# Kernel optimization log

Hardware: AMD Instinct MI355X
Metric: run time of the kernel (lower is better)

The kernel has to match this reference:

```python
import jax, jax.numpy as jnp
import numpy as np

N_USERS = 100000
N_ITEMS = 200000
N_TOTAL = N_USERS + N_ITEMS
N_EDGES = 6000000
D = 64


def setup_inputs() -> dict:
    key = jax.random.key(0)
    ks = jax.random.split(key, 7)
    A_row = jax.random.randint(ks[0], (N_EDGES,), 0, N_TOTAL, dtype=jnp.int32)
    A_col = jax.random.randint(ks[1], (N_EDGES,), 0, N_TOTAL, dtype=jnp.int32)
    A_val = jax.random.uniform(ks[2], (N_EDGES,), dtype=jnp.float32)
    user_feat = jax.random.normal(ks[3], (N_USERS, D), dtype=jnp.float32)
    item_feat = jax.random.normal(ks[4], (N_ITEMS, D), dtype=jnp.float32)
    W = jax.random.normal(ks[5], (D, D), dtype=jnp.float32) * (6.0 / (D + D)) ** 0.5
    b = jnp.zeros((D,), dtype=jnp.float32)
    return {"A_row": A_row, "A_col": A_col, "A_val": A_val,
            "user_feat": user_feat, "item_feat": item_feat, "W": W, "b": b}


def reference(A_row, A_col, A_val, user_feat, item_feat, W, b):
    # fc applied to users and items (same weight), then concat -> [N_total, D]
    all_feat = jnp.concatenate([user_feat, item_feat], axis=0)
    trans = all_feat @ W.T + b  # nn.Linear: x @ W^T + b
    # sparse A (COO) @ trans: gather source rows, scale by edge value, scatter-add to dest
    msgs = A_val[:, None] * trans[A_col]  # [E, D]
    conv = jax.ops.segment_sum(msgs, A_row, num_segments=N_TOTAL)  # [N_total, D]
    # identity residual (in_dim == out_dim)
    out = conv + all_feat
    return out[:N_USERS], out[N_USERS:]
```

## Files before the change

kernel.cpp:

```cpp
#include <hip/hip_runtime.h>
#include <hip/hip_fp16.h>

#define N_USERS 100000
#define N_ITEMS 200000
#define N_TOTAL 300000
#define N_EDGES 6000000
#define D 64

#define B2SHIFT 10
#define B2ROWS 1024
#define NBUCK2 ((N_TOTAL + B2ROWS - 1) / B2ROWS)
#define CAP 22016
#define EPB 8192
#define NPB ((N_EDGES + EPB - 1) / EPB)

#define VSCALE 8191.0f
#define VINV   (1.0f / 8191.0f)

typedef float    f32x4 __attribute__((ext_vector_type(4)));
typedef float    f32x2 __attribute__((ext_vector_type(2)));
typedef _Float16 f16x8 __attribute__((ext_vector_type(8)));

#define LIN_BLOCKS ((N_TOTAL + 63) / 64)

__global__ __launch_bounds__(256) void fused_lin_part_kernel(
    const float* __restrict__ user_feat,
    const float* __restrict__ item_feat,
    const float* __restrict__ W,
    const float* __restrict__ bias,
    __half* __restrict__ trans,
    const int*   __restrict__ A_row,
    const int*   __restrict__ A_col,
    const float* __restrict__ A_val,
    int*  __restrict__ gcur,
    int2* __restrict__ kv)
{
    if (blockIdx.x < NPB) {
        __shared__ int lcnt[NBUCK2];
        __shared__ int gb[NBUCK2];
        for (int i = threadIdx.x; i < NBUCK2; i += 256) lcnt[i] = 0;
        __syncthreads();

        const int base = blockIdx.x * EPB;
        int pk[32];
        #pragma unroll
        for (int j = 0; j < 8; ++j) {
            const int e0 = base + j * 1024 + threadIdx.x * 4;
            if (e0 < N_EDGES) {
                const int4 r = *reinterpret_cast<const int4*>(A_row + e0);
                pk[4*j+0] = ((r.x >> B2SHIFT) << 13) | atomicAdd(&lcnt[r.x >> B2SHIFT], 1);
                pk[4*j+1] = ((r.y >> B2SHIFT) << 13) | atomicAdd(&lcnt[r.y >> B2SHIFT], 1);
                pk[4*j+2] = ((r.z >> B2SHIFT) << 13) | atomicAdd(&lcnt[r.z >> B2SHIFT], 1);
                pk[4*j+3] = ((r.w >> B2SHIFT) << 13) | atomicAdd(&lcnt[r.w >> B2SHIFT], 1);
            }
        }
        __syncthreads();
        for (int i = threadIdx.x; i < NBUCK2; i += 256)
            gb[i] = lcnt[i] ? atomicAdd(&gcur[i], lcnt[i]) : 0;
        __syncthreads();

        #pragma unroll
        for (int j = 0; j < 8; ++j) {
            const int e0 = base + j * 1024 + threadIdx.x * 4;
            if (e0 < N_EDGES) {
                const int4   r = *reinterpret_cast<const int4*>(A_row + e0);
                const int4   c = *reinterpret_cast<const int4*>(A_col + e0);
                const float4 v = *reinterpret_cast<const float4*>(A_val + e0);
                const int rr[4] = {r.x, r.y, r.z, r.w};
                const int cc[4] = {c.x, c.y, c.z, c.w};
                const float vv[4] = {v.x, v.y, v.z, v.w};
                #pragma unroll
                for (int q = 0; q < 4; ++q) {
                    const int p   = pk[4*j+q];
                    const int bk  = p >> 13;
                    const int pos = gb[bk] + (p & 0x1FFF);
                    if (pos < CAP) {
                        kv[(size_t)bk * CAP + pos] = make_int2(
                            ((rr[q] & (B2ROWS - 1)) << 19) | cc[q],
                            __float_as_int(vv[q]));
                    }
                }
            }
        }
    } else {
        const int bid  = blockIdx.x - NPB;
        const int lane = threadIdx.x & 63;
        const int wv   = threadIdx.x >> 6;
        const int r0   = bid * 64 + wv * 16;
        const int arow = lane & 15;
        const int kg   = lane >> 4;

        f16x8 wf[4][2];
        #pragma unroll
        for (int ct = 0; ct < 4; ++ct) {
            const float* wp = W + (size_t)(ct * 16 + arow) * D;
            #pragma unroll
            for (int kf = 0; kf < 2; ++kf) {
                const int k0 = kf * 32 + kg * 8;
                const float4 w0 = *reinterpret_cast<const float4*>(wp + k0);
                const float4 w1 = *reinterpret_cast<const float4*>(wp + k0 + 4);
                f16x8 h;
                h[0] = (_Float16)w0.x; h[1] = (_Float16)w0.y;
                h[2] = (_Float16)w0.z; h[3] = (_Float16)w0.w;
                h[4] = (_Float16)w1.x; h[5] = (_Float16)w1.y;
                h[6] = (_Float16)w1.z; h[7] = (_Float16)w1.w;
                wf[ct][kf] = h;
            }
        }

        int rr = r0 + arow;
        if (rr >= N_TOTAL) rr = N_TOTAL - 1;
        const float* fp = (rr < N_USERS) ? user_feat + (size_t)rr * D
                                         : item_feat + (size_t)(rr - N_USERS) * D;
        f16x8 af[2];
        #pragma unroll
        for (int kf = 0; kf < 2; ++kf) {
            const int k0 = kf * 32 + kg * 8;
            const float4 a0 = *reinterpret_cast<const float4*>(fp + k0);
            const float4 a1 = *reinterpret_cast<const float4*>(fp + k0 + 4);
            f16x8 h;
            h[0] = (_Float16)a0.x; h[1] = (_Float16)a0.y;
            h[2] = (_Float16)a0.z; h[3] = (_Float16)a0.w;
            h[4] = (_Float16)a1.x; h[5] = (_Float16)a1.y;
            h[6] = (_Float16)a1.z; h[7] = (_Float16)a1.w;
            af[kf] = h;
        }

        #pragma unroll
        for (int ct = 0; ct < 4; ++ct) {
            const float bc = bias[ct * 16 + arow];
            f32x4 acc = {bc, bc, bc, bc};
            acc = __builtin_amdgcn_mfma_f32_16x16x32_f16(af[0], wf[ct][0], acc, 0, 0, 0);
            acc = __builtin_amdgcn_mfma_f32_16x16x32_f16(af[1], wf[ct][1], acc, 0, 0, 0);
            #pragma unroll
            for (int reg = 0; reg < 4; ++reg) {
                const int ro = r0 + kg * 4 + reg;
                if (ro < N_TOTAL)
                    trans[(size_t)ro * D + ct * 16 + arow] = __float2half(acc[reg]);
            }
        }
    }
}

__global__ __launch_bounds__(512) void bucket_csr3_kernel(
    const int*  __restrict__ gcur,
    const int2* __restrict__ kv,
    int* __restrict__ rowoff,
    int* __restrict__ outp)
{
    __shared__ int rcnt[B2ROWS];
    __shared__ int rcur[B2ROWS];
    __shared__ int s[512];
    const int b    = blockIdx.x;
    const int t    = threadIdx.x;
    const int n    = min(gcur[b], CAP);
    const int base = b * CAP;

    rcnt[t] = 0; rcnt[t + 512] = 0;
    __syncthreads();
    for (int i = t; i < n; i += 512)
        atomicAdd(&rcnt[kv[base + i].x >> 19], 1);
    __syncthreads();

    const int v0 = rcnt[t * 2], v1 = rcnt[t * 2 + 1];
    s[t] = v0 + v1;
    __syncthreads();
    for (int d2 = 1; d2 < 512; d2 <<= 1) {
        const int x = (t >= d2) ? s[t - d2] : 0;
        __syncthreads();
        s[t] += x;
        __syncthreads();
    }
    const int run = (t == 0) ? 0 : s[t - 1];
    rcur[t * 2]     = run;
    rcur[t * 2 + 1] = run + v0;
    __syncthreads();

    for (int i = t; i < n; i += 512) {
        const int2 e = kv[base + i];
        const int  p = atomicAdd(&rcur[e.x >> 19], 1);
        const int  q = (int)fminf(fmaxf(__int_as_float(e.y) * VSCALE + 0.5f, 0.0f), VSCALE);
        outp[base + p] = (q << 19) | (e.x & 0x7FFFF);
    }
    __syncthreads();

    const int rbase = b << B2SHIFT;
    for (int i = t; i < B2ROWS; i += 512) {
        const int row = rbase + i;
        if (row < N_TOTAL) rowoff[row] = base + rcur[i];
    }
}

__global__ __launch_bounds__(256) void pull6_kernel(
    const int*    __restrict__ rowoff,
    const int*    __restrict__ outp,
    const __half* __restrict__ trans,
    const float*  __restrict__ user_feat,
    const float*  __restrict__ item_feat,
    float* __restrict__ out)
{
    const int lane = threadIdx.x & 63;
    const int row  = blockIdx.x * 4 + (threadIdx.x >> 6);
    if (row >= N_TOTAL) return;
    const int g  = lane >> 3;
    const int l8 = lane & 7;

    const int s0 = ((row & (B2ROWS - 1)) == 0) ? (row >> B2SHIFT) * CAP
                                               : rowoff[row - 1];
    const int e  = rowoff[row];

    f32x2 a0 = {0.f, 0.f}, a1 = {0.f, 0.f}, a2 = {0.f, 0.f}, a3 = {0.f, 0.f};
    f32x2 b0 = {0.f, 0.f}, b1 = {0.f, 0.f}, b2 = {0.f, 0.f}, b3 = {0.f, 0.f};

    for (int bi = s0; bi < e; bi += 16) {
        const int i0 = bi + g;
        const int i1 = bi + 8 + g;
        const int k0 = (i0 < e) ? outp[i0] : 0;
        const int k1 = (i1 < e) ? outp[i1] : 0;

        const float4 gv0 = *reinterpret_cast<const float4*>(
            trans + ((size_t)(k0 & 0x7FFFF) << 6) + 8 * l8);
        const float4 gv1 = *reinterpret_cast<const float4*>(
            trans + ((size_t)(k1 & 0x7FFFF) << 6) + 8 * l8);

        const float w0 = (float)((unsigned)k0 >> 19) * VINV;
        const float w1 = (float)((unsigned)k1 >> 19) * VINV;
        const f32x2 w20 = {w0, w0};
        const f32x2 w21 = {w1, w1};

        const float2 f00 = __half22float2(*reinterpret_cast<const __half2*>(&gv0.x));
        const float2 f01 = __half22float2(*reinterpret_cast<const __half2*>(&gv0.y));
        const float2 f02 = __half22float2(*reinterpret_cast<const __half2*>(&gv0.z));
        const float2 f03 = __half22float2(*reinterpret_cast<const __half2*>(&gv0.w));
        a0 += w20 * (f32x2){f00.x, f00.y};
        a1 += w20 * (f32x2){f01.x, f01.y};
        a2 += w20 * (f32x2){f02.x, f02.y};
        a3 += w20 * (f32x2){f03.x, f03.y};

        const float2 f10 = __half22float2(*reinterpret_cast<const __half2*>(&gv1.x));
        const float2 f11 = __half22float2(*reinterpret_cast<const __half2*>(&gv1.y));
        const float2 f12 = __half22float2(*reinterpret_cast<const __half2*>(&gv1.z));
        const float2 f13 = __half22float2(*reinterpret_cast<const __half2*>(&gv1.w));
        b0 += w21 * (f32x2){f10.x, f10.y};
        b1 += w21 * (f32x2){f11.x, f11.y};
        b2 += w21 * (f32x2){f12.x, f12.y};
        b3 += w21 * (f32x2){f13.x, f13.y};
    }

    a0 += b0; a1 += b1; a2 += b2; a3 += b3;

    #pragma unroll
    for (int d2 = 8; d2 <= 32; d2 <<= 1) {
        a0[0] += __shfl_xor(a0[0], d2); a0[1] += __shfl_xor(a0[1], d2);
        a1[0] += __shfl_xor(a1[0], d2); a1[1] += __shfl_xor(a1[1], d2);
        a2[0] += __shfl_xor(a2[0], d2); a2[1] += __shfl_xor(a2[1], d2);
        a3[0] += __shfl_xor(a3[0], d2); a3[1] += __shfl_xor(a3[1], d2);
    }

    if (g == 0) {
        const float* fp = (row < N_USERS)
            ? user_feat + ((size_t)row << 6)
            : item_feat + ((size_t)(row - N_USERS) << 6);
        const float4 r0 = *reinterpret_cast<const float4*>(fp + 8 * l8);
        const float4 r1 = *reinterpret_cast<const float4*>(fp + 8 * l8 + 4);
        float* op = out + ((size_t)row << 6) + 8 * l8;
        *reinterpret_cast<float4*>(op) =
            make_float4(a0[0] + r0.x, a0[1] + r0.y, a1[0] + r0.z, a1[1] + r0.w);
        *reinterpret_cast<float4*>(op + 4) =
            make_float4(a2[0] + r1.x, a2[1] + r1.y, a3[0] + r1.z, a3[1] + r1.w);
    }
}

__global__ __launch_bounds__(256) void linear_kernel(
    const float* __restrict__ user_feat,
    const float* __restrict__ item_feat,
    const float* __restrict__ W,
    const float* __restrict__ b,
    float* __restrict__ trans,
    float* __restrict__ out)
{
    __shared__ float Ws[D][D + 1];
    __shared__ float bs[D];
    const int t = threadIdx.x;
    for (int i = t; i < D * D; i += 256) Ws[i >> 6][i & 63] = W[i];
    if (t < D) bs[t] = b[t];
    __syncthreads();

    const int lane = t & 63;
    const int row  = blockIdx.x * 4 + (t >> 6);
    if (row >= N_TOTAL) return;

    const float* feat = (row < N_USERS)
        ? user_feat + (size_t)row * D
        : item_feat + (size_t)(row - N_USERS) * D;

    const float fv = feat[lane];
    float acc = bs[lane];
    #pragma unroll
    for (int k = 0; k < D; ++k)
        acc = fmaf(__shfl(fv, k, 64), Ws[lane][k], acc);

    const size_t off = (size_t)row * D + lane;
    trans[off] = acc;
    if (out) out[off] = fv;
}

__global__ __launch_bounds__(256) void edge_scatter_kernel(
    const int*   __restrict__ A_row,
    const int*   __restrict__ A_col,
    const float* __restrict__ A_val,
    const float* __restrict__ trans,
    float*       __restrict__ out)
{
    const int lane = threadIdx.x & 63;
    const long long e = ((long long)blockIdx.x * 256 + threadIdx.x) >> 6;
    if (e >= N_EDGES) return;
    atomicAdd(out + (size_t)A_row[e] * D + lane,
              A_val[e] * trans[(size_t)A_col[e] * D + lane]);
}

__global__ __launch_bounds__(256) void init_out_kernel(
    const float* __restrict__ user_feat,
    const float* __restrict__ item_feat,
    float* __restrict__ out)
{
    const size_t i = (size_t)blockIdx.x * 256 + threadIdx.x;
    if (i >= (size_t)N_TOTAL * D) return;
    const size_t urows = (size_t)N_USERS * D;
    out[i] = (i < urows) ? user_feat[i] : item_feat[i - urows];
}

__global__ __launch_bounds__(256) void fused_edge_kernel(
    const int*   __restrict__ A_row,
    const int*   __restrict__ A_col,
    const float* __restrict__ A_val,
    const float* __restrict__ user_feat,
    const float* __restrict__ item_feat,
    const float* __restrict__ W,
    const float* __restrict__ b,
    float*       __restrict__ out)
{
    __shared__ float Ws[D][D + 1];
    __shared__ float bs[D];
    const int t = threadIdx.x;
    for (int i = t; i < D * D; i += 256) Ws[i >> 6][i & 63] = W[i];
    if (t < D) bs[t] = b[t];
    __syncthreads();

    const int lane = t & 63;
    const long long e = ((long long)blockIdx.x * 256 + t) >> 6;
    if (e >= N_EDGES) return;

    const int   r = A_row[e];
    const int   c = A_col[e];
    const float v = A_val[e];

    const float* feat = (c < N_USERS)
        ? user_feat + (size_t)c * D
        : item_feat + (size_t)(c - N_USERS) * D;

    const float fv = feat[lane];
    float acc = bs[lane];
    #pragma unroll
    for (int k = 0; k < D; ++k)
        acc = fmaf(__shfl(fv, k, 64), Ws[lane][k], acc);

    atomicAdd(out + (size_t)r * D + lane, v * acc);
}

extern "C" void kernel_launch(void* const* d_in, const int* in_sizes, int n_in,
                              void* d_out, int out_size, void* d_ws, size_t ws_size,
                              hipStream_t stream)
{
    const int*   A_row     = (const int*)  d_in[0];
    const int*   A_col     = (const int*)  d_in[1];
    const float* A_val     = (const float*)d_in[2];
    const float* user_feat = (const float*)d_in[3];
    const float* item_feat = (const float*)d_in[4];
    const float* W         = (const float*)d_in[5];
    const float* b         = (const float*)d_in[6];
    float*       out       = (float*)d_out;

    const size_t a256 = 255;
    const size_t transh_bytes = (((size_t)N_TOTAL * D * sizeof(__half)) + a256) & ~a256;
    const size_t gcur_bytes   = (((size_t)NBUCK2 * sizeof(int)) + a256) & ~a256;
    const size_t kv_bytes     = (((size_t)NBUCK2 * CAP * sizeof(int2)) + a256) & ~a256;
    const size_t rowoff_bytes = (((size_t)N_TOTAL * sizeof(int)) + a256) & ~a256;
    const size_t outp_bytes   = (((size_t)NBUCK2 * CAP * sizeof(int)) + a256) & ~a256;
    const size_t main_total   = transh_bytes + gcur_bytes + kv_bytes
                              + rowoff_bytes + outp_bytes;

    const size_t trans_bytes  = (size_t)N_TOTAL * D * sizeof(float);

    const int row_blocks = (N_TOTAL + 3) / 4;

    if (ws_size >= main_total) {
        char* p = (char*)d_ws;
        __half* transh = (__half*)p;  p += transh_bytes;
        int*    gcur   = (int*)p;     p += gcur_bytes;
        int2*   kv     = (int2*)p;    p += kv_bytes;
        int*    rowoff = (int*)p;     p += rowoff_bytes;
        int*    outp   = (int*)p;

        hipMemsetAsync(gcur, 0, (size_t)NBUCK2 * sizeof(int), stream);
        fused_lin_part_kernel<<<NPB + LIN_BLOCKS, 256, 0, stream>>>(
            user_feat, item_feat, W, b, transh,
            A_row, A_col, A_val, gcur, kv);
        bucket_csr3_kernel<<<NBUCK2, 512, 0, stream>>>(
            gcur, kv, rowoff, outp);
        pull6_kernel<<<row_blocks, 256, 0, stream>>>(
            rowoff, outp, transh, user_feat, item_feat, out);
    } else if (ws_size >= trans_bytes) {
        float* trans = (float*)d_ws;
        linear_kernel<<<row_blocks, 256, 0, stream>>>(
            user_feat, item_feat, W, b, trans, out);
        edge_scatter_kernel<<<N_EDGES / 4, 256, 0, stream>>>(
            A_row, A_col, A_val, trans, out);
    } else {
        const size_t total = (size_t)N_TOTAL * D;
        init_out_kernel<<<(int)((total + 255) / 256), 256, 0, stream>>>(
            user_feat, item_feat, out);
        fused_edge_kernel<<<N_EDGES / 4, 256, 0, stream>>>(
            A_row, A_col, A_val, user_feat, item_feat, W, b, out);
    }
}
```

Measured before the change: 365.7 us.

## Stage partitioned edges in LDS for contiguous per-bucket global writes

Result: faster. 329.4 us (-9.9%).

```diff
diff --git a/kernel.cpp b/kernel.cpp
--- a/kernel.cpp
+++ b/kernel.cpp
@@ -11,7 +11,7 @@
 #define B2ROWS 1024
 #define NBUCK2 ((N_TOTAL + B2ROWS - 1) / B2ROWS)
 #define CAP 22016
-#define EPB 8192
+#define EPB 4096
 #define NPB ((N_EDGES + EPB - 1) / EPB)
 
 #define VSCALE 8191.0f
@@ -35,17 +35,22 @@
     int*  __restrict__ gcur,
     int2* __restrict__ kv)
 {
+    __shared__ int  lcnt[NBUCK2];
+    __shared__ int  gb[NBUCK2];
+    __shared__ int  loff[NBUCK2 + 1];
+    __shared__ int  s[256];
+    __shared__ int2 stage[EPB];
+
     if (blockIdx.x < NPB) {
-        __shared__ int lcnt[NBUCK2];
-        __shared__ int gb[NBUCK2];
-        for (int i = threadIdx.x; i < NBUCK2; i += 256) lcnt[i] = 0;
+        const int t = threadIdx.x;
+        for (int i = t; i < NBUCK2; i += 256) lcnt[i] = 0;
         __syncthreads();
 
         const int base = blockIdx.x * EPB;
-        int pk[32];
+        int pk[16];
         #pragma unroll
-        for (int j = 0; j < 8; ++j) {
-            const int e0 = base + j * 1024 + threadIdx.x * 4;
+        for (int j = 0; j < 4; ++j) {
+            const int e0 = base + j * 1024 + t * 4;
             if (e0 < N_EDGES) {
                 const int4 r = *reinterpret_cast<const int4*>(A_row + e0);
                 pk[4*j+0] = ((r.x >> B2SHIFT) << 13) | atomicAdd(&lcnt[r.x >> B2SHIFT], 1);
@@ -55,13 +60,28 @@
             }
         }
         __syncthreads();
-        for (int i = threadIdx.x; i < NBUCK2; i += 256)
+
+        const int i0 = t * 2, i1 = t * 2 + 1;
+        const int v0 = (i0 < NBUCK2) ? lcnt[i0] : 0;
+        const int v1 = (i1 < NBUCK2) ? lcnt[i1] : 0;
+        s[t] = v0 + v1;
+        __syncthreads();
+        for (int d2 = 1; d2 < 256; d2 <<= 1) {
+            const int x = (t >= d2) ? s[t - d2] : 0;
+            __syncthreads();
+            s[t] += x;
+            __syncthreads();
+        }
+        const int run = (t == 0) ? 0 : s[t - 1];
+        if (i0 < NBUCK2) loff[i0] = run;
+        if (i1 < NBUCK2) loff[i1] = run + v0;
+        for (int i = t; i < NBUCK2; i += 256)
             gb[i] = lcnt[i] ? atomicAdd(&gcur[i], lcnt[i]) : 0;
         __syncthreads();
 
         #pragma unroll
-        for (int j = 0; j < 8; ++j) {
-            const int e0 = base + j * 1024 + threadIdx.x * 4;
+        for (int j = 0; j < 4; ++j) {
+            const int e0 = base + j * 1024 + t * 4;
             if (e0 < N_EDGES) {
                 const int4   r = *reinterpret_cast<const int4*>(A_row + e0);
                 const int4   c = *reinterpret_cast<const int4*>(A_col + e0);
@@ -71,15 +91,26 @@
                 const float vv[4] = {v.x, v.y, v.z, v.w};
                 #pragma unroll
                 for (int q = 0; q < 4; ++q) {
-                    const int p   = pk[4*j+q];
-                    const int bk  = p >> 13;
-                    const int pos = gb[bk] + (p & 0x1FFF);
-                    if (pos < CAP) {
-                        kv[(size_t)bk * CAP + pos] = make_int2(
-                            ((rr[q] & (B2ROWS - 1)) << 19) | cc[q],
-                            __float_as_int(vv[q]));
-                    }
+                    const int p  = pk[4*j+q];
+                    const int bk = p >> 13;
+                    stage[loff[bk] + (p & 0x1FFF)] = make_int2(
+                        ((rr[q] & (B2ROWS - 1)) << 19) | cc[q],
+                        __float_as_int(vv[q]));
                 }
+            }
+        }
+        __syncthreads();
+
+        const int wv   = t >> 6;
+        const int lane = t & 63;
+        for (int b2 = wv; b2 < NBUCK2; b2 += 4) {
+            const int st    = loff[b2];
+            const int len   = lcnt[b2];
+            const int gbase = gb[b2];
+            int2* dst = kv + (size_t)b2 * CAP;
+            for (int j = lane; j < len; j += 64) {
+                const int pos = gbase + j;
+                if (pos < CAP) dst[pos] = stage[st + j];
             }
         }
     } else {
```
